# Performance work log

Measured on AMD Instinct MI355X. Metric: run time of the kernel, lower is better.

The kernel has to match this reference:

```python
import jax, jax.numpy as jnp
import numpy as np

BITWIDTH = 8
T = 1 << BITWIDTH          # bit-stream length = 2**bitwidth = 256
B = 16                     # independent unary streams
IN1, H1, H2, OUT = 1024, 512, 256, 10


def sobol_rng(bitwidth=BITWIDTH):
    # 1-D unscrambled Sobol sequence (== torch.quasirandom.SobolEngine(1)),
    n = 1 << bitwidth
    i = np.arange(n, dtype=np.uint32)
    g = i ^ (i >> 1)  # Gray code
    x = np.zeros(n, dtype=np.float64)
    for j in range(bitwidth):
        x += ((g >> np.uint32(j)) & np.uint32(1)).astype(np.float64) * 2.0 ** -(j + 1)
    return jnp.asarray(x * 2.0 - 1.0, dtype=jnp.float32)


def _forward(w1, b1, w2, b2, w3, b3, prediction, x):
    rng = sobol_rng()
    f32 = jnp.float32
    Bn = x.shape[1]

    def lin_state(fin, fout):
        # rng_wght_idx rows are all identical in the torch code (the [1, fin]
        # input broadcasts across [fout, fin]), so we keep only [B, fin].
        return (jnp.zeros((Bn, fin), jnp.int32),   # rng_wght_idx
                jnp.zeros((Bn, fin), jnp.int32),   # rng_wght_idx_inv
                jnp.zeros((Bn, fout), f32),        # in_accumulator
                jnp.zeros((Bn, fout), f32))        # out_accumulator

    def ulinear(state, xf, xi, w, bvec, t, offset):
        cum, cum_inv, in_acc, out_acc = state
        # regenerate binary weight matrices by compare against gathered rng
        w_pos = (w[None, :, :] > rng[cum][:, None, :]).astype(f32)      # [B, fout, fin]
        w_neg = (w[None, :, :] <= rng[cum_inv][:, None, :]).astype(f32)  # [B, fout, fin]
        bias_bit = (bvec > rng[t]).astype(f32)                           # [fout]
        y = (jnp.einsum('bi,boi->bo', xf, w_pos)
             + jnp.einsum('bi,boi->bo', 1.0 - xf, w_neg)
             + bias_bit[None, :])
        in_acc = in_acc + y - offset
        out = (in_acc > out_acc).astype(f32)
        out_acc = out_acc + out
        return (cum + xi, cum_inv + (1 - xi), in_acc, out_acc), out

    def ucompare(acc, inp):  # unary ReLU (UnaryCompare)
        sign = (acc < 0).astype(f32)
        out = sign + (1.0 - sign) * inp
        return acc + 2.0 * out - 1.0, out

    def step(carry, xs_t):
        s1, c1, s2, c2, s3 = carry
        xi, t = xs_t
        xf = xi.astype(f32)
        s1, y1 = ulinear(s1, xf, xi, w1, b1, t, (IN1 - 1) / 2)
        c1, a1 = ucompare(c1, y1)
        s2, y2 = ulinear(s2, a1, a1.astype(jnp.int32), w2, b2, t, (H1 - 1) / 2)
        c2, a2 = ucompare(c2, y2)
        s3, y3 = ulinear(s3, a2, a2.astype(jnp.int32), w3, b3, t, (H2 - 1) / 2)
        # ProgressivePrecision is re-created every forward: out_pp = 2*y3 - 1,
        # err = out_pp - prediction, then log_softmax.
        out_t = jax.nn.log_softmax(2.0 * y3 - 1.0 - prediction, axis=1)
        return (s1, c1, s2, c2, s3), out_t

    init = (lin_state(IN1, H1), jnp.zeros((Bn, H1), f32),
            lin_state(H1, H2), jnp.zeros((Bn, H2), f32),
            lin_state(H2, OUT))
    _, outs = jax.lax.scan(step, init, (x, jnp.arange(T)))
    return outs  # [T, B, OUT]


def setup_inputs():
    key = jax.random.key(0)
    ks = jax.random.split(key, 8)
    u = lambda k, s: jax.random.uniform(k, s, jnp.float32, -1.0, 1.0)
    return {
        'w1': u(ks[0], (H1, IN1)), 'b1': u(ks[1], (H1,)),
        'w2': u(ks[2], (H2, H1)), 'b2': u(ks[3], (H2,)),
        'w3': u(ks[4], (OUT, H2)), 'b3': u(ks[5], (OUT,)),
        'prediction': 0.1 * jax.random.normal(ks[6], (B, OUT), jnp.float32),
        'x': jax.random.randint(ks[7], (T, B, IN1), 0, 2, jnp.int32),
    }


def reference(w1, b1, w2, b2, w3, b3, prediction, x):
    return _forward(w1, b1, w2, b2, w3, b3, prediction, x)
```

## Files before the change

kernel.cpp:

```cpp
#include <hip/hip_runtime.h>
#include <stdint.h>

#define TSTEPS 256
#define NB 16
#define NM (TSTEPS*NB)

typedef short s16x2 __attribute__((ext_vector_type(2)));

__device__ __forceinline__ uint32_t perm8(int i) {
  uint32_t g = (uint32_t)(i ^ (i >> 1));
  return __brev(g) >> 24;
}

__device__ __forceinline__ void qmad(uint32_t& z, uint32_t a, uint32_t t_s,
                                     uint32_t e) {
  asm("v_pk_mad_i16 %0, %1, %2, %3" : "=v"(z) : "v"(a), "s"(t_s), "v"(e));
}
__device__ __forceinline__ uint32_t qperm(uint32_t x, uint32_t y, uint32_t sel) {
  uint32_t d;
  asm("v_perm_b32 %0, %1, %2, %3" : "=v"(d) : "v"(x), "v"(y), "v"(sel));
  return d;
}
__device__ __forceinline__ void qsad(uint32_t& acc, uint32_t p) {
  asm("v_sad_u8 %0, %1, 0, %0" : "+v"(acc) : "v"(p));
}

__device__ __forceinline__ void qstep3(uint32_t& acc, uint32_t t2, uint32_t a2,
                                       uint32_t e2, uint32_t c15) {
  uint32_t z;
  asm("v_pk_mad_i16 %0, %2, %3, %4\n\t"
      "v_pk_ashrrev_i16 %0, %5, %0\n\t"
      "v_pk_add_i16 %1, %1, %0"
      : "=&v"(z), "+v"(acc)
      : "v"(a2), "v"(t2), "v"(e2), "v"(c15));
}

__device__ __forceinline__ uint32_t pkadd16(uint32_t a, uint32_t b) {
  return __builtin_bit_cast(uint32_t,
        (s16x2)(__builtin_bit_cast(s16x2, a) + __builtin_bit_cast(s16x2, b)));
}

__device__ __forceinline__ void unpackAE(uint32_t v2, uint32_t& a2, uint32_t& e2) {
  s16x2 sv = __builtin_bit_cast(s16x2, v2) >> 15;
  uint32_t su = __builtin_bit_cast(uint32_t, sv);
  uint32_t vand = v2 & 0x01FF01FFu;
  e2 = pkadd16(~vand, su & 0x01FF01FFu);
  a2 = pkadd16(0x00010001u, pkadd16(su, su));
}

__device__ __forceinline__ int rank256(float w) {
  double v = 128.0 * (double)w + 128.0;
  int t = (int)ceil(v);
  if (t < 0) t = 0; if (t > 256) t = 256;
  return t;
}

#define SUMLOHI(A,B,C,D, LO, HI) \
  LO = (A & 0xFFFFu) + (B & 0xFFFFu) + (C & 0xFFFFu) + (D & 0xFFFFu); \
  HI = (A >> 16) + (B >> 16) + (C >> 16) + (D >> 16);

__global__ __launch_bounds__(256) void k_prepA(
    const float* __restrict__ w1, const float* __restrict__ w2,
    const float* __restrict__ w3, const float* __restrict__ b1,
    const float* __restrict__ b2, const float* __restrict__ b3,
    const int* __restrict__ x,
    uint32_t* __restrict__ T1, uint32_t* __restrict__ T2,
    uint32_t* __restrict__ T3t, uint32_t* __restrict__ bb1,
    uint32_t* __restrict__ bb2, uint32_t* __restrict__ bb3,
    uint16_t* __restrict__ cs)
{
  int bid = blockIdx.x, tid = threadIdx.x;
  if (bid < 1024) {
    int e = bid * 256 + tid;
    int n = e >> 9, kp = e & 511;
    int dst = ((kp >> 2) * 512 + n) * 4 + (kp & 3);
    T1[dst] = (uint32_t)rank256(w1[2 * e]) |
              ((uint32_t)rank256(w1[2 * e + 1]) << 16);
  } else if (bid < 1280) {
    int e = (bid - 1024) * 256 + tid;
    int n = e >> 8, kp = e & 255;
    int dst = ((kp >> 2) * 256 + n) * 4 + (kp & 3);
    T2[dst] = (uint32_t)rank256(w2[2 * e]) |
              ((uint32_t)rank256(w2[2 * e + 1]) << 16);
  } else if (bid < 1285) {
    int e = (bid - 1280) * 256 + tid;
    if (e < 1280) {
      int n = e % 10, kp = e / 10;
      T3t[e] = (uint32_t)rank256(w3[n * 256 + 2 * kp]) |
               ((uint32_t)rank256(w3[n * 256 + 2 * kp + 1]) << 16);
    }
  } else if (bid < 1301) {
    int w = (bid - 1285) * 256 + tid;
    int o = w >> 3, j = w & 7;
    double bv = (double)b1[o] * 128.0 + 128.0;
    uint32_t bits = 0;
    for (int s = 0; s < 32; ++s)
      if (bv > (double)perm8(j * 32 + s)) bits |= 1u << s;
    bb1[w] = bits;
  } else if (bid < 1309) {
    int w = (bid - 1301) * 256 + tid;
    int o = w >> 3, j = w & 7;
    double bv = (double)b2[o] * 128.0 + 128.0;
    uint32_t bits = 0;
    for (int s = 0; s < 32; ++s)
      if (bv > (double)perm8(j * 32 + s)) bits |= 1u << s;
    bb2[w] = bits;
  } else if (bid == 1309) {
    if (tid < 80) {
      int o = tid >> 3, j = tid & 7;
      double bv = (double)b3[o] * 128.0 + 128.0;
      uint32_t bits = 0;
      for (int s = 0; s < 32; ++s)
        if (bv > (double)perm8(j * 32 + s)) bits |= 1u << s;
      bb3[tid] = bits;
    }
  } else {
    int g = (bid - 1310) * 256 + tid;
    int i = g & 1023, b = (g >> 10) & 15, c = g >> 14;
    int s = 0, t0 = c * 32;
    for (int tt = t0; tt < t0 + 32; ++tt)
      s += x[((size_t)tt * NB + b) * 1024 + i];
    cs[(c * NB + b) * 1024 + i] = (uint16_t)s;
  }
}

__global__ __launch_bounds__(256) void k_prep1ae(const int* __restrict__ x,
                                                 const uint16_t* __restrict__ cs,
                                                 uint2* __restrict__ AE1) {
  int g = blockIdx.x * 256 + threadIdx.x;
  int ip = g & 511;
  int b = (g >> 9) & 15, c = g >> 13;
  int i0 = 2 * ip;
  int cum0 = 0, cum1 = 0;
  for (int cc = 0; cc < c; ++cc) {
    uint32_t two = *(const uint32_t*)(cs + (cc * NB + b) * 1024 + i0);
    cum0 += (int)(two & 0xFFFFu);
    cum1 += (int)(two >> 16);
  }
  int t0 = c * 32;
  for (int tt = t0; tt < t0 + 32; ++tt) {
    int m = b * 256 + tt;
    int2 xv = *(const int2*)(x + ((size_t)tt * NB + b) * 1024 + i0);
    int idx0 = xv.x ? cum0 : (tt - cum0);
    int idx1 = xv.y ? cum1 : (tt - cum1);
    uint32_t p0 = perm8(idx0), p1 = perm8(idx1);
    uint32_t v0 = (xv.x ? p0 : (510u - p0)) | ((uint32_t)(xv.x ^ 1) << 15);
    uint32_t v1 = (xv.y ? p1 : (510u - p1)) | ((uint32_t)(xv.y ^ 1) << 15);
    uint32_t a2, e2;
    unpackAE(v0 | (v1 << 16), a2, e2);
    AE1[(size_t)m * 512 + ip] = make_uint2(a2, e2);
    cum0 += xv.x; cum1 += xv.y;
  }
}

template<int KD, int NT, int NREG, int KC>
__global__ __launch_bounds__(256, 4) void k_gemmv6(
    const uint2* __restrict__ AE, const uint32_t* __restrict__ T,
    uint16_t* __restrict__ Yp)
{
  const int tid = threadIdx.x;
  const int m = blockIdx.x * 256 + tid;
  const int n0 = blockIdx.y * NREG;
  const int sk = blockIdx.z;
  const int k0 = sk * KC;
  uint32_t sel = 0x07050301u;
  uint32_t acc[NREG];
  #pragma unroll
  for (int nn = 0; nn < NREG; ++nn) acc[nn] = 0;
  const uint4* vsrc = (const uint4*)(AE + (size_t)m * (KD / 2) + (k0 >> 1));
  const uint32_t* tcbase = T + ((size_t)(k0 >> 3) * NT + n0) * 4;
  #pragma unroll 1
  for (int c = 0; c < KC / 8; ++c) {
    uint4 w01 = vsrc[2 * c];
    uint4 w23 = vsrc[2 * c + 1];
    uint32_t a0 = w01.x, e0 = w01.y, a1 = w01.z, e1 = w01.w;
    uint32_t a2v = w23.x, e2v = w23.y, a3 = w23.z, e3 = w23.w;
    asm volatile("" : "+v"(a0), "+v"(e0), "+v"(a1), "+v"(e1),
                      "+v"(a2v), "+v"(e2v), "+v"(a3), "+v"(e3));
    const uint4* tcp = (const uint4*)(tcbase + (size_t)c * NT * 4);
    uint4 tw[NREG];
    #pragma unroll
    for (int nn = 0; nn < NREG; ++nn) tw[nn] = tcp[nn];
    #pragma unroll
    for (int nn = 0; nn < NREG; ++nn) {
      uint32_t z0, z1, z2, z3;
      qmad(z0, a0, tw[nn].x, e0);
      qmad(z1, a1, tw[nn].y, e1);
      qmad(z2, a2v, tw[nn].z, e2v);
      qmad(z3, a3, tw[nn].w, e3);
      qsad(acc[nn], qperm(z0, z1, sel));
      qsad(acc[nn], qperm(z2, z3, sel));
    }
  }
  uint16_t* outp = Yp + ((size_t)sk * NT + n0) * (size_t)NM + m;
  #pragma unroll
  for (int nn = 0; nn < NREG; ++nn)
    outp[(size_t)nn * NM] = (uint16_t)acc[nn];
}

template<int KD, int NT, int NREG, int KC>
__global__ __launch_bounds__(256, 4) void k_gemmv6b(
    const uint16_t* __restrict__ A, const uint16_t* __restrict__ E,
    const uint32_t* __restrict__ T, uint16_t* __restrict__ Yp)
{
  const int tid = threadIdx.x;
  const int m = blockIdx.x * 256 + tid;
  const int n0 = blockIdx.y * NREG;
  const int sk = blockIdx.z;
  const int k0 = sk * KC;
  uint32_t sel = 0x07050301u;
  uint32_t acc[NREG];
  #pragma unroll
  for (int nn = 0; nn < NREG; ++nn) acc[nn] = 0;
  const uint4* asrc = (const uint4*)(A + (size_t)m * KD + k0);
  const uint4* esrc = (const uint4*)(E + (size_t)m * KD + k0);
  const uint32_t* tcbase = T + ((size_t)(k0 >> 3) * NT + n0) * 4;
  #pragma unroll 1
  for (int c = 0; c < KC / 8; ++c) {
    uint4 aw = asrc[c];
    uint4 ew = esrc[c];
    uint32_t a0 = aw.x, a1 = aw.y, a2v = aw.z, a3 = aw.w;
    uint32_t e0 = ew.x, e1 = ew.y, e2v = ew.z, e3 = ew.w;
    asm volatile("" : "+v"(a0), "+v"(e0), "+v"(a1), "+v"(e1),
                      "+v"(a2v), "+v"(e2v), "+v"(a3), "+v"(e3));
    const uint4* tcp = (const uint4*)(tcbase + (size_t)c * NT * 4);
    uint4 tw[NREG];
    #pragma unroll
    for (int nn = 0; nn < NREG; ++nn) tw[nn] = tcp[nn];
    #pragma unroll
    for (int nn = 0; nn < NREG; ++nn) {
      uint32_t z0, z1, z2, z3;
      qmad(z0, a0, tw[nn].x, e0);
      qmad(z1, a1, tw[nn].y, e1);
      qmad(z2, a2v, tw[nn].z, e2v);
      qmad(z3, a3, tw[nn].w, e3);
      qsad(acc[nn], qperm(z0, z1, sel));
      qsad(acc[nn], qperm(z2, z3, sel));
    }
  }
  uint16_t* outp = Yp + ((size_t)sk * NT + n0) * (size_t)NM + m;
  #pragma unroll
  for (int nn = 0; nn < NREG; ++nn)
    outp[(size_t)nn * NM] = (uint16_t)acc[nn];
}

template<int NOUT, int KD, int OFF2, int LOGN>
__global__ __launch_bounds__(64) void k_scanv4(
    const uint16_t* __restrict__ Yp, const uint32_t* __restrict__ bb,
    uint16_t* __restrict__ Aout, uint16_t* __restrict__ Eout)
{
  const size_t PS = (size_t)NOUT * NM;
  int g = blockIdx.x * 64 + threadIdx.x;
  int o = g & (NOUT - 1);
  int b = g >> LOGN;
  const uint16_t* row = Yp + (size_t)o * NM + b * 256;
  const int C = 255 * (2 * KD - OFF2);
  int inA = 0, outA = 0, cA = 0, cum = 0;
  uint4 c0 = *(const uint4*)(row);
  uint4 c1 = *(const uint4*)(row + PS);
  uint4 c2 = *(const uint4*)(row + 2 * PS);
  uint4 c3 = *(const uint4*)(row + 3 * PS);
  #pragma unroll
  for (int w = 0; w < 8; ++w) {
    uint32_t bwc = bb[o * 8 + w];
    #pragma unroll
    for (int cchunk = 0; cchunk < 4; ++cchunk) {
      int t0 = w * 32 + cchunk * 8;
      uint4 n0v = c0, n1v = c1, n2v = c2, n3v = c3;
      if (t0 < 248) {
        n0v = *(const uint4*)(row + t0 + 8);
        n1v = *(const uint4*)(row + PS + t0 + 8);
        n2v = *(const uint4*)(row + 2 * PS + t0 + 8);
        n3v = *(const uint4*)(row + 3 * PS + t0 + 8);
      }
      uint32_t s[8];
      SUMLOHI(c0.x, c1.x, c2.x, c3.x, s[0], s[1]);
      SUMLOHI(c0.y, c1.y, c2.y, c3.y, s[2], s[3]);
      SUMLOHI(c0.z, c1.z, c2.z, c3.z, s[4], s[5]);
      SUMLOHI(c0.w, c1.w, c2.w, c3.w, s[6], s[7]);
      #pragma unroll
      for (int j = 0; j < 8; ++j) {
        int t = t0 + j;
        int bit = (int)((bwc >> (t & 31)) & 1u);
        inA += C + 510 * bit - 2 * (int)s[j];
        int outb = (inA > outA) ? 1 : 0;
        outA += 510 * outb;
        int a = (cA < 0) ? 1 : outb;
        cA += 1020 * a - 510;
        int idx = a ? cum : (t - cum);
        cum += a;
        uint32_t p = perm8(idx);
        size_t off = (size_t)(b * 256 + t) * NOUT + o;
        Aout[off] = a ? (uint16_t)1 : (uint16_t)0xFFFF;
        Eout[off] = a ? (uint16_t)(~p) : (uint16_t)p;
      }
      c0 = n0v; c1 = n1v; c2 = n2v; c3 = n3v;
    }
  }
}

__global__ __launch_bounds__(256) void k_l3(
    const uint16_t* __restrict__ A3, const uint16_t* __restrict__ E3,
    const uint32_t* __restrict__ T3t, uint16_t* __restrict__ y3t)
{
  __shared__ uint32_t T3s[128][16];
  __shared__ uint32_t UFs3[16][258];
  int tid = threadIdx.x;
  int m0 = blockIdx.x * 16;
  const uint32_t c15 = 0x000F000Fu;
  for (int j = tid; j < 2048; j += 256) {
    int kp = j >> 4, o2 = j & 15;
    T3s[kp][o2] = (o2 < 10) ? T3t[kp * 10 + o2] : 0u;
  }
  { int row = tid >> 4, part = tid & 15;
    const uint4* as = (const uint4*)(A3 + (size_t)(m0 + row) * 256 + part * 16);
    const uint4* es = (const uint4*)(E3 + (size_t)(m0 + row) * 256 + part * 16);
    uint4 aA = as[0], aB = as[1];
    uint4 eA = es[0], eB = es[1];
    uint32_t o[16] = {aA.x, eA.x, aA.y, eA.y, aA.z, eA.z, aA.w, eA.w,
                      aB.x, eB.x, aB.y, eB.y, aB.z, eB.z, aB.w, eB.w};
    #pragma unroll
    for (int q4 = 0; q4 < 4; ++q4)
      *(uint4*)&UFs3[row][part * 16 + q4 * 4] =
          make_uint4(o[q4 * 4], o[q4 * 4 + 1], o[q4 * 4 + 2], o[q4 * 4 + 3]);
  }
  __syncthreads();
  int mr = tid >> 4, o = tid & 15;
  uint32_t acc = 0;
  #pragma unroll 4
  for (int kp2 = 0; kp2 < 64; ++kp2) {
    uint4 uf = *(const uint4*)&UFs3[mr][kp2 * 4];
    qstep3(acc, T3s[2 * kp2][o],     uf.x, uf.y, c15);
    qstep3(acc, T3s[2 * kp2 + 1][o], uf.z, uf.w, c15);
  }
  if (o < 10) {
    int mm = m0 + mr;
    int b = mm >> 8, t = mm & 255;
    y3t[(size_t)(b * 16 + o) * 256 + t] =
        (uint16_t)(256 + (short)(acc & 0xFFFFu) + (short)(acc >> 16));
  }
}

__global__ __launch_bounds__(256) void k_scan3sm(
    const uint16_t* __restrict__ y3t, const uint32_t* __restrict__ bb3,
    const float* __restrict__ pred, float* __restrict__ out)
{
  __shared__ uint32_t obl[16][16][8];
  __shared__ float prs[160];
  int tid = threadIdx.x;
  if (tid < 160) prs[tid] = pred[tid];
  int b = tid >> 4, o = tid & 15;
  if (o < 10) {
    const uint16_t* row = y3t + (size_t)(b * 16 + o) * 256;
    int in2 = 0, out2 = 0;
    uint4 cur = *(const uint4*)row;
    #pragma unroll
    for (int w = 0; w < 8; ++w) {
      uint32_t bwc = bb3[o * 8 + w];
      uint32_t bits = 0;
      #pragma unroll
      for (int cchunk = 0; cchunk < 4; ++cchunk) {
        int t0 = w * 32 + cchunk * 8;
        uint4 nxt = cur;
        if (t0 < 248) nxt = *(const uint4*)(row + t0 + 8);
        uint32_t cw[4] = {cur.x, cur.y, cur.z, cur.w};
        #pragma unroll
        for (int j = 0; j < 8; ++j) {
          int t = t0 + j;
          int cnt = (int)((cw[j >> 1] >> ((j & 1) * 16)) & 0xFFFFu);
          in2 += 2 * cnt + 2 * (int)((bwc >> (t & 31)) & 1u) - 255;
          int outb = (in2 > out2) ? 1 : 0;
          out2 += outb << 1;
          bits |= (uint32_t)outb << (t & 31);
        }
        cur = nxt;
      }
      obl[b][o][w] = bits;
    }
  }
  __syncthreads();
  for (int r = tid; r < 4096; r += 256) {
    int t = r >> 4, b2 = r & 15;
    float z[10], mx = -3e38f;
    #pragma unroll
    for (int oo = 0; oo < 10; ++oo) {
      int bit = (obl[b2][oo][t >> 5] >> (t & 31)) & 1;
      z[oo] = (bit ? 1.f : -1.f) - prs[b2 * 10 + oo];
      mx = fmaxf(mx, z[oo]);
    }
    float s = 0.f;
    #pragma unroll
    for (int oo = 0; oo < 10; ++oo) s += expf(z[oo] - mx);
    float ls = logf(s);
    float* op = out + (size_t)r * 10;
    #pragma unroll
    for (int oo = 0; oo < 10; ++oo) op[oo] = z[oo] - mx - ls;
  }
}

extern "C" void kernel_launch(void* const* d_in, const int* in_sizes, int n_in,
                              void* d_out, int out_size, void* d_ws, size_t ws_size,
                              hipStream_t stream) {
  (void)in_sizes; (void)n_in; (void)out_size; (void)ws_size;
  const float* w1   = (const float*)d_in[0];
  const float* b1   = (const float*)d_in[1];
  const float* w2   = (const float*)d_in[2];
  const float* b2   = (const float*)d_in[3];
  const float* w3   = (const float*)d_in[4];
  const float* b3   = (const float*)d_in[5];
  const float* pred = (const float*)d_in[6];
  const int*   x    = (const int*)d_in[7];
  float* out = (float*)d_out;
  uint8_t* W = (uint8_t*)d_ws;

  uint32_t* T1   = (uint32_t*)(W + 0);
  uint32_t* T2   = (uint32_t*)(W + 1048576);
  uint32_t* T3t  = (uint32_t*)(W + 1310720);
  uint32_t* bb1  = (uint32_t*)(W + 1318912);
  uint32_t* bb2  = (uint32_t*)(W + 1335296);
  uint32_t* bb3  = (uint32_t*)(W + 1343488);
  uint16_t* chks = (uint16_t*)(W + 1344000);
  uint2*    AE1  = (uint2*)   (W + 1606144);
  uint16_t* Yp1  = (uint16_t*)(W + 18383360);
  uint16_t* A2   = (uint16_t*)(W + 1606144);
  uint16_t* E2   = (uint16_t*)(W + 5800448);
  uint16_t* A3   = (uint16_t*)(W + 9994752);
  uint16_t* E3   = (uint16_t*)(W + 12091904);
  uint16_t* y3t  = (uint16_t*)(W + 14189056);
  uint16_t* Yp2  = Yp1;

  hipLaunchKernelGGL(k_prepA, dim3(1822), dim3(256), 0, stream,
                     w1, w2, w3, b1, b2, b3, x, T1, T2, T3t, bb1, bb2, bb3, chks);
  hipLaunchKernelGGL(k_prep1ae, dim3(256), dim3(256), 0, stream, x, chks, AE1);
  hipLaunchKernelGGL((k_gemmv6<1024, 512, 16, 256>), dim3(16, 32, 4), dim3(256),
                     0, stream, AE1, T1, Yp1);
  hipLaunchKernelGGL((k_scanv4<512, 1024, 1023, 9>), dim3(128), dim3(64), 0,
                     stream, Yp1, bb1, A2, E2);
  hipLaunchKernelGGL((k_gemmv6b<512, 256, 16, 128>), dim3(16, 16, 4), dim3(256),
                     0, stream, A2, E2, T2, Yp2);
  hipLaunchKernelGGL((k_scanv4<256, 512, 511, 8>), dim3(64), dim3(64), 0,
                     stream, Yp2, bb2, A3, E3);
  hipLaunchKernelGGL(k_l3, dim3(256), dim3(256), 0, stream, A3, E3, T3t, y3t);
  hipLaunchKernelGGL(k_scan3sm, dim3(1), dim3(256), 0, stream, y3t, bb3, pred, out);
}
```

Before: 209.5 us.

## Pack scan outputs into one 16-bit word and compute two rows per thread in layer-1 GEMM

The scan kernels now write a single packed 16-bit value per element instead of separate A and E arrays. The layer-2 GEMM and layer-3 kernel unpack it on the fly, which halves the intermediate traffic in exchange for extra ALU unpack work. The layer-1 GEMM now has each thread process two M rows, 2048 apart, sharing each loaded T tile, and launches half as many blocks. This reuses the T loads across rows but doubles accumulator registers and may lower occupancy.

New measurement: 200.8 us. 4.2% less time.

```diff
diff --git a/kernel.cpp b/kernel.cpp
--- a/kernel.cpp
+++ b/kernel.cpp
@@ -154,8 +154,67 @@
 }
 
 template<int KD, int NT, int NREG, int KC>
-__global__ __launch_bounds__(256, 4) void k_gemmv6(
+__global__ __launch_bounds__(256, 4) void k_gemmv7(
     const uint2* __restrict__ AE, const uint32_t* __restrict__ T,
+    uint16_t* __restrict__ Yp)
+{
+  const int tid = threadIdx.x;
+  const int m0 = blockIdx.x * 256 + tid;
+  const int m1 = m0 + 2048;
+  const int n0 = blockIdx.y * NREG;
+  const int sk = blockIdx.z;
+  const int k0 = sk * KC;
+  uint32_t sel = 0x07050301u;
+  uint32_t accA[NREG], accB[NREG];
+  #pragma unroll
+  for (int nn = 0; nn < NREG; ++nn) { accA[nn] = 0; accB[nn] = 0; }
+  const uint4* vsrc0 = (const uint4*)(AE + (size_t)m0 * (KD / 2) + (k0 >> 1));
+  const uint4* vsrc1 = (const uint4*)(AE + (size_t)m1 * (KD / 2) + (k0 >> 1));
+  const uint32_t* tcbase = T + ((size_t)(k0 >> 3) * NT + n0) * 4;
+  #pragma unroll 1
+  for (int c = 0; c < KC / 8; ++c) {
+    uint4 wa01 = vsrc0[2 * c], wa23 = vsrc0[2 * c + 1];
+    uint4 wb01 = vsrc1[2 * c], wb23 = vsrc1[2 * c + 1];
+    uint32_t a0 = wa01.x, e0 = wa01.y, a1 = wa01.z, e1 = wa01.w;
+    uint32_t a2v = wa23.x, e2v = wa23.y, a3 = wa23.z, e3 = wa23.w;
+    uint32_t f0 = wb01.x, g0 = wb01.y, f1 = wb01.z, g1 = wb01.w;
+    uint32_t f2 = wb23.x, g2 = wb23.y, f3 = wb23.z, g3 = wb23.w;
+    asm volatile("" : "+v"(a0), "+v"(e0), "+v"(a1), "+v"(e1),
+                      "+v"(a2v), "+v"(e2v), "+v"(a3), "+v"(e3),
+                      "+v"(f0), "+v"(g0), "+v"(f1), "+v"(g1),
+                      "+v"(f2), "+v"(g2), "+v"(f3), "+v"(g3));
+    const uint4* tcp = (const uint4*)(tcbase + (size_t)c * NT * 4);
+    uint4 tw[NREG];
+    #pragma unroll
+    for (int nn = 0; nn < NREG; ++nn) tw[nn] = tcp[nn];
+    #pragma unroll
+    for (int nn = 0; nn < NREG; ++nn) {
+      uint32_t z0, z1, z2, z3;
+      qmad(z0, a0, tw[nn].x, e0);
+      qmad(z1, a1, tw[nn].y, e1);
+      qmad(z2, a2v, tw[nn].z, e2v);
+      qmad(z3, a3, tw[nn].w, e3);
+      qsad(accA[nn], qperm(z0, z1, sel));
+      qsad(accA[nn], qperm(z2, z3, sel));
+      qmad(z0, f0, tw[nn].x, g0);
+      qmad(z1, f1, tw[nn].y, g1);
+      qmad(z2, f2, tw[nn].z, g2);
+      qmad(z3, f3, tw[nn].w, g3);
+      qsad(accB[nn], qperm(z0, z1, sel));
+      qsad(accB[nn], qperm(z2, z3, sel));
+    }
+  }
+  uint16_t* outp = Yp + ((size_t)sk * NT + n0) * (size_t)NM;
+  #pragma unroll
+  for (int nn = 0; nn < NREG; ++nn) {
+    outp[(size_t)nn * NM + m0] = (uint16_t)accA[nn];
+    outp[(size_t)nn * NM + m1] = (uint16_t)accB[nn];
+  }
+}
+
+template<int KD, int NT, int NREG, int KC>
+__global__ __launch_bounds__(256, 4) void k_gemmv5c(
+    const uint16_t* __restrict__ V, const uint32_t* __restrict__ T,
     uint16_t* __restrict__ Yp)
 {
   const int tid = threadIdx.x;
@@ -167,14 +226,16 @@
   uint32_t acc[NREG];
   #pragma unroll
   for (int nn = 0; nn < NREG; ++nn) acc[nn] = 0;
-  const uint4* vsrc = (const uint4*)(AE + (size_t)m * (KD / 2) + (k0 >> 1));
+  const uint4* vsrc = (const uint4*)(V + (size_t)m * KD + k0);
   const uint32_t* tcbase = T + ((size_t)(k0 >> 3) * NT + n0) * 4;
   #pragma unroll 1
   for (int c = 0; c < KC / 8; ++c) {
-    uint4 w01 = vsrc[2 * c];
-    uint4 w23 = vsrc[2 * c + 1];
-    uint32_t a0 = w01.x, e0 = w01.y, a1 = w01.z, e1 = w01.w;
-    uint32_t a2v = w23.x, e2v = w23.y, a3 = w23.z, e3 = w23.w;
+    uint4 vv = vsrc[c];
+    uint32_t a0, e0, a1, e1, a2v, e2v, a3, e3;
+    unpackAE(vv.x, a0, e0);
+    unpackAE(vv.y, a1, e1);
+    unpackAE(vv.z, a2v, e2v);
+    unpackAE(vv.w, a3, e3);
     asm volatile("" : "+v"(a0), "+v"(e0), "+v"(a1), "+v"(e1),
                       "+v"(a2v), "+v"(e2v), "+v"(a3), "+v"(e3));
     const uint4* tcp = (const uint4*)(tcbase + (size_t)c * NT * 4);
@@ -198,56 +259,10 @@
     outp[(size_t)nn * NM] = (uint16_t)acc[nn];
 }
 
-template<int KD, int NT, int NREG, int KC>
-__global__ __launch_bounds__(256, 4) void k_gemmv6b(
-    const uint16_t* __restrict__ A, const uint16_t* __restrict__ E,
-    const uint32_t* __restrict__ T, uint16_t* __restrict__ Yp)
-{
-  const int tid = threadIdx.x;
-  const int m = blockIdx.x * 256 + tid;
-  const int n0 = blockIdx.y * NREG;
-  const int sk = blockIdx.z;
-  const int k0 = sk * KC;
-  uint32_t sel = 0x07050301u;
-  uint32_t acc[NREG];
-  #pragma unroll
-  for (int nn = 0; nn < NREG; ++nn) acc[nn] = 0;
-  const uint4* asrc = (const uint4*)(A + (size_t)m * KD + k0);
-  const uint4* esrc = (const uint4*)(E + (size_t)m * KD + k0);
-  const uint32_t* tcbase = T + ((size_t)(k0 >> 3) * NT + n0) * 4;
-  #pragma unroll 1
-  for (int c = 0; c < KC / 8; ++c) {
-    uint4 aw = asrc[c];
-    uint4 ew = esrc[c];
-    uint32_t a0 = aw.x, a1 = aw.y, a2v = aw.z, a3 = aw.w;
-    uint32_t e0 = ew.x, e1 = ew.y, e2v = ew.z, e3 = ew.w;
-    asm volatile("" : "+v"(a0), "+v"(e0), "+v"(a1), "+v"(e1),
-                      "+v"(a2v), "+v"(e2v), "+v"(a3), "+v"(e3));
-    const uint4* tcp = (const uint4*)(tcbase + (size_t)c * NT * 4);
-    uint4 tw[NREG];
-    #pragma unroll
-    for (int nn = 0; nn < NREG; ++nn) tw[nn] = tcp[nn];
-    #pragma unroll
-    for (int nn = 0; nn < NREG; ++nn) {
-      uint32_t z0, z1, z2, z3;
-      qmad(z0, a0, tw[nn].x, e0);
-      qmad(z1, a1, tw[nn].y, e1);
-      qmad(z2, a2v, tw[nn].z, e2v);
-      qmad(z3, a3, tw[nn].w, e3);
-      qsad(acc[nn], qperm(z0, z1, sel));
-      qsad(acc[nn], qperm(z2, z3, sel));
-    }
-  }
-  uint16_t* outp = Yp + ((size_t)sk * NT + n0) * (size_t)NM + m;
-  #pragma unroll
-  for (int nn = 0; nn < NREG; ++nn)
-    outp[(size_t)nn * NM] = (uint16_t)acc[nn];
-}
-
 template<int NOUT, int KD, int OFF2, int LOGN>
-__global__ __launch_bounds__(64) void k_scanv4(
+__global__ __launch_bounds__(64) void k_scanv3(
     const uint16_t* __restrict__ Yp, const uint32_t* __restrict__ bb,
-    uint16_t* __restrict__ Aout, uint16_t* __restrict__ Eout)
+    uint16_t* __restrict__ Vn)
 {
   const size_t PS = (size_t)NOUT * NM;
   int g = blockIdx.x * 64 + threadIdx.x;
@@ -290,9 +305,8 @@
         int idx = a ? cum : (t - cum);
         cum += a;
         uint32_t p = perm8(idx);
-        size_t off = (size_t)(b * 256 + t) * NOUT + o;
-        Aout[off] = a ? (uint16_t)1 : (uint16_t)0xFFFF;
-        Eout[off] = a ? (uint16_t)(~p) : (uint16_t)p;
+        Vn[(size_t)(b * 256 + t) * NOUT + o] =
+            (uint16_t)((a ? p : (510u - p)) | ((uint32_t)(a ^ 1) << 15));
       }
       c0 = n0v; c1 = n1v; c2 = n2v; c3 = n3v;
     }
@@ -300,8 +314,8 @@
 }
 
 __global__ __launch_bounds__(256) void k_l3(
-    const uint16_t* __restrict__ A3, const uint16_t* __restrict__ E3,
-    const uint32_t* __restrict__ T3t, uint16_t* __restrict__ y3t)
+    const uint16_t* __restrict__ V3, const uint32_t* __restrict__ T3t,
+    uint16_t* __restrict__ y3t)
 {
   __shared__ uint32_t T3s[128][16];
   __shared__ uint32_t UFs3[16][258];
@@ -313,12 +327,12 @@
     T3s[kp][o2] = (o2 < 10) ? T3t[kp * 10 + o2] : 0u;
   }
   { int row = tid >> 4, part = tid & 15;
-    const uint4* as = (const uint4*)(A3 + (size_t)(m0 + row) * 256 + part * 16);
-    const uint4* es = (const uint4*)(E3 + (size_t)(m0 + row) * 256 + part * 16);
-    uint4 aA = as[0], aB = as[1];
-    uint4 eA = es[0], eB = es[1];
-    uint32_t o[16] = {aA.x, eA.x, aA.y, eA.y, aA.z, eA.z, aA.w, eA.w,
-                      aB.x, eB.x, aB.y, eB.y, aB.z, eB.z, aB.w, eB.w};
+    const uint4* src = (const uint4*)(V3 + (size_t)(m0 + row) * 256 + part * 16);
+    uint4 pa = src[0], pb = src[1];
+    uint32_t w[8] = {pa.x, pa.y, pa.z, pa.w, pb.x, pb.y, pb.z, pb.w};
+    uint32_t o[16];
+    #pragma unroll
+    for (int q = 0; q < 8; ++q) unpackAE(w[q], o[q * 2], o[q * 2 + 1]);
     #pragma unroll
     for (int q4 = 0; q4 < 4; ++q4)
       *(uint4*)&UFs3[row][part * 16 + q4 * 4] =
@@ -422,24 +436,22 @@
   uint16_t* chks = (uint16_t*)(W + 1344000);
   uint2*    AE1  = (uint2*)   (W + 1606144);
   uint16_t* Yp1  = (uint16_t*)(W + 18383360);
-  uint16_t* A2   = (uint16_t*)(W + 1606144);
-  uint16_t* E2   = (uint16_t*)(W + 5800448);
-  uint16_t* A3   = (uint16_t*)(W + 9994752);
-  uint16_t* E3   = (uint16_t*)(W + 12091904);
-  uint16_t* y3t  = (uint16_t*)(W + 14189056);
+  uint16_t* V2   = (uint16_t*)(W + 1606144);
+  uint16_t* V3   = (uint16_t*)(W + 5800448);
+  uint16_t* y3t  = (uint16_t*)(W + 7897600);
   uint16_t* Yp2  = Yp1;
 
   hipLaunchKernelGGL(k_prepA, dim3(1822), dim3(256), 0, stream,
                      w1, w2, w3, b1, b2, b3, x, T1, T2, T3t, bb1, bb2, bb3, chks);
   hipLaunchKernelGGL(k_prep1ae, dim3(256), dim3(256), 0, stream, x, chks, AE1);
-  hipLaunchKernelGGL((k_gemmv6<1024, 512, 16, 256>), dim3(16, 32, 4), dim3(256),
+  hipLaunchKernelGGL((k_gemmv7<1024, 512, 16, 256>), dim3(8, 32, 4), dim3(256),
                      0, stream, AE1, T1, Yp1);
-  hipLaunchKernelGGL((k_scanv4<512, 1024, 1023, 9>), dim3(128), dim3(64), 0,
-                     stream, Yp1, bb1, A2, E2);
-  hipLaunchKernelGGL((k_gemmv6b<512, 256, 16, 128>), dim3(16, 16, 4), dim3(256),
-                     0, stream, A2, E2, T2, Yp2);
-  hipLaunchKernelGGL((k_scanv4<256, 512, 511, 8>), dim3(64), dim3(64), 0,
-                     stream, Yp2, bb2, A3, E3);
-  hipLaunchKernelGGL(k_l3, dim3(256), dim3(256), 0, stream, A3, E3, T3t, y3t);
+  hipLaunchKernelGGL((k_scanv3<512, 1024, 1023, 9>), dim3(128), dim3(64), 0,
+                     stream, Yp1, bb1, V2);
+  hipLaunchKernelGGL((k_gemmv5c<512, 256, 16, 128>), dim3(16, 16, 4), dim3(256),
+                     0, stream, V2, T2, Yp2);
+  hipLaunchKernelGGL((k_scanv3<256, 512, 511, 8>), dim3(64), dim3(64), 0,
+                     stream, Yp2, bb2, V3);
+  hipLaunchKernelGGL(k_l3, dim3(256), dim3(256), 0, stream, V3, T3t, y3t);
   hipLaunchKernelGGL(k_scan3sm, dim3(1), dim3(256), 0, stream, y3t, bb3, pred, out);
 }
```
